# Performance work log

Hardware: AMD Instinct MI355X
Metric: run time of the kernel (lower is better)

Reference implementation:

```python
import jax, jax.numpy as jnp
import numpy as np

D = 384
EPS = 1e-12  # F.normalize eps


def setup_inputs() -> dict:
    key = jax.random.key(0)
    ks = jax.random.split(key, 12)
    s = 1.0 / np.sqrt(D)  # torch Linear default init scale
    return {
        "x": jax.random.normal(ks[0], (8192, D), jnp.float32),
        "y": jax.random.normal(ks[1], (8192, D), jnp.float32),
        "Wq": jax.random.uniform(ks[2], (D, D), jnp.float32, -s, s),
        "bq": jax.random.uniform(ks[3], (D,), jnp.float32, -s, s),
        "Wk": jax.random.uniform(ks[4], (D, D), jnp.float32, -s, s),
        "bk": jax.random.uniform(ks[5], (D,), jnp.float32, -s, s),
        "Wv": jax.random.uniform(ks[6], (D, D), jnp.float32, -s, s),
        "bv": jax.random.uniform(ks[7], (D,), jnp.float32, -s, s),
        "Wo": jax.random.uniform(ks[8], (D, D), jnp.float32, -s, s),
        "bo": jax.random.uniform(ks[9], (D,), jnp.float32, -s, s),
    }


def reference(x, y, Wq, bq, Wk, bk, Wv, bv, Wo, bo):
    # Q: [N, d], K/V: [M, d]
    Q = x @ Wq.T + bq
    K = y @ Wk.T + bk
    V = y @ Wv.T + bv
    scale = 1.0 / jnp.sqrt(jnp.asarray(Q.shape[-1], Q.dtype))
    attn = jax.nn.softmax((Q @ K.T) * scale, axis=-1)  # [N, M]
    ctx = attn @ V  # [N, d]
    # F.normalize(p=2, dim=1): divide by max(||row||_2, eps)
    norm = jnp.maximum(jnp.linalg.norm(ctx, axis=1, keepdims=True), EPS)
    ctx = ctx / norm
    return (x + ctx) @ Wo.T + bo
```

## Files before the change

### kernel.cpp

```cpp
#include <hip/hip_runtime.h>
#include <stdint.h>


typedef __attribute__((ext_vector_type(8))) short bf16x8;
typedef __attribute__((ext_vector_type(4))) float f32x4;
typedef __attribute__((ext_vector_type(16))) float f32x16;

#define DEV static __device__ __forceinline__

DEV short f2bf(float f) {
  uint32_t u = __builtin_bit_cast(uint32_t, f);
  u += 0x7fffu + ((u >> 16) & 1u);
  return (short)(u >> 16);
}
DEV uint32_t pack2(float a, float b) {
  return (uint32_t)(uint16_t)f2bf(a) | ((uint32_t)(uint16_t)f2bf(b) << 16);
}
DEV unsigned cvt_pk(float lo, float hi) {
  unsigned r;
  asm("v_cvt_pk_bf16_f32 %0, %1, %2" : "=v"(r) : "v"(lo), "v"(hi));
  return r;
}
DEV void pl32swap(unsigned& a, unsigned& b) {
  asm volatile("v_permlane32_swap_b32 %0, %1" : "+v"(a), "+v"(b));
}
DEV void gload16(const void* g, void* l) {
  __builtin_amdgcn_global_load_lds(
      (const __attribute__((address_space(1))) unsigned*)g,
      (__attribute__((address_space(3))) unsigned*)l, 16, 0, 0);
}

template <int BIAS_ON_N, int OUT_F32, int A_F32>
__global__ __launch_bounds__(256) void gemm_nt(
    const void* __restrict__ Aptr, const float* __restrict__ B,
    const float* __restrict__ bias, void* __restrict__ Cptr,
    int M, int N, int K, float scale) {
  __shared__ char As[128 * 128];
  __shared__ char Bs[128 * 128];
  const int tid = threadIdx.x;
  const int l = tid & 63, w = tid >> 6;
  const int lq = l & 15, lk = l >> 4;
  const int m0 = blockIdx.x * 128, n0 = blockIdx.y * 128;
  const int wr = (w >> 1) * 64, wc = (w & 1) * 64;
  f32x4 acc[4][4] = {};

  for (int k0 = 0; k0 < K; k0 += 64) {
    if (A_F32) {
      const float* A = (const float*)Aptr;
#pragma unroll
      for (int i = 0; i < 8; i++) {
        int c = tid + i * 256;
        int row = c >> 4, col = (c & 15) * 4;
        f32x4 v = *(const f32x4*)(A + (size_t)(m0 + row) * K + k0 + col);
        uint32_t lo = pack2(v.x, v.y), hi = pack2(v.z, v.w);
        int off = (row * 128 + col * 2) ^ ((row & 7) << 4);
        *(uint32_t*)(As + off) = lo;
        *(uint32_t*)(As + off + 4) = hi;
      }
    } else {
      const short* A = (const short*)Aptr;
#pragma unroll
      for (int i = 0; i < 4; i++) {
        int c = tid + i * 256;
        int row = c >> 3, col = (c & 7) * 8;
        uint4 v = *(const uint4*)(A + (size_t)(m0 + row) * K + k0 + col);
        int off = (row * 128 + col * 2) ^ ((row & 7) << 4);
        *(uint4*)(As + off) = v;
      }
    }
#pragma unroll
    for (int i = 0; i < 8; i++) {
      int c = tid + i * 256;
      int row = c >> 4, col = (c & 15) * 4;
      f32x4 v = *(const f32x4*)(B + (size_t)(n0 + row) * K + k0 + col);
      uint32_t lo = pack2(v.x, v.y), hi = pack2(v.z, v.w);
      int off = (row * 128 + col * 2) ^ ((row & 7) << 4);
      *(uint32_t*)(Bs + off) = lo;
      *(uint32_t*)(Bs + off + 4) = hi;
    }
    __syncthreads();
#pragma unroll
    for (int ks = 0; ks < 2; ks++) {
      bf16x8 af[4], bfr[4];
#pragma unroll
      for (int m = 0; m < 4; m++) {
        int row = wr + m * 16 + lq;
        af[m] = *(const bf16x8*)(As + ((row * 128 + ks * 64 + lk * 16) ^ ((row & 7) << 4)));
      }
#pragma unroll
      for (int n = 0; n < 4; n++) {
        int row = wc + n * 16 + lq;
        bfr[n] = *(const bf16x8*)(Bs + ((row * 128 + ks * 64 + lk * 16) ^ ((row & 7) << 4)));
      }
#pragma unroll
      for (int m = 0; m < 4; m++)
#pragma unroll
        for (int n = 0; n < 4; n++)
          acc[m][n] = __builtin_amdgcn_mfma_f32_16x16x32_bf16(af[m], bfr[n], acc[m][n], 0, 0, 0);
    }
    __syncthreads();
  }
#pragma unroll
  for (int m = 0; m < 4; m++) {
    int mg = m0 + wr + m * 16 + lk * 4;
#pragma unroll
    for (int n = 0; n < 4; n++) {
      int ng = n0 + wc + n * 16 + lq;
#pragma unroll
      for (int r = 0; r < 4; r++) {
        float v = (acc[m][n][r] + (BIAS_ON_N ? bias[ng] : bias[mg + r])) * scale;
        if (OUT_F32)
          ((float*)Cptr)[(size_t)(mg + r) * N + ng] = v;
        else
          ((short*)Cptr)[(size_t)(mg + r) * N + ng] = f2bf(v);
      }
    }
  }
}

#define ITERS 64

__global__ __launch_bounds__(256)
__attribute__((amdgpu_waves_per_eu(2, 2))) void flash_attn(
    const short* __restrict__ Qb, const short* __restrict__ Kb,
    const short* __restrict__ Vt, float* __restrict__ ctx_part) {
  __shared__ char Ks[2][24576];
  __shared__ char Vs[24576];
  const int tid = threadIdx.x, l = tid & 63, w = tid >> 6;
  const int l31 = l & 31, h = l >> 5;
  const int qh = w >> 1, dh = w & 1;
  const int sp = blockIdx.x & 3, qt = blockIdx.x >> 2;
  const int q0 = qt * 64 + qh * 32;
  const int kvbase = sp * 2048;

  int koff[6], voff[6];
#pragma unroll
  for (int i = 0; i < 6; i++) {
    int d = (w * 6 + i) * 1024 + l * 16;
    int krow = d / 768, kc = d - krow * 768;
    koff[i] = krow * 768 + (kc ^ ((krow & 7) << 4));
    int vrow = d >> 6, vc = d & 63;
    voff[i] = vrow * 16384 + (vc ^ (((vrow >> 1) & 3) << 4));
  }
  const int ldsoff = w * 6144 + 0;

  bf16x8 qf[24];
  {
    const short* qrow = Qb + (size_t)(q0 + l31) * 384 + h * 8;
#pragma unroll
    for (int s = 0; s < 24; s++) qf[s] = *(const bf16x8*)(qrow + s * 16);
  }
  asm volatile("s_waitcnt vmcnt(0)" ::: "memory");

  {
    const char* kb = (const char*)Kb + (size_t)kvbase * 768;
#pragma unroll
    for (int i = 0; i < 6; i++)
      gload16(kb + koff[i], (char*)Ks[0] + ldsoff + i * 1024);
  }

  f32x16 acc[6] = {};

#pragma unroll 1
  for (int t = 0; t < ITERS; t++) {
    const char* Kc = Ks[t & 1];
    {
      const char* vb = (const char*)Vt + (size_t)(kvbase + t * 32) * 2;
#pragma unroll
      for (int i = 0; i < 6; i++)
        gload16(vb + voff[i], Vs + ldsoff + i * 1024);
    }
    asm volatile("s_waitcnt vmcnt(6)" ::: "memory");
    __builtin_amdgcn_s_barrier();

    f32x16 S = {};
    const char* kcb = Kc + l31 * 768;
    const int swzk = (l31 & 7) << 4;
    __builtin_amdgcn_s_setprio(1);
#pragma unroll
    for (int s = 0; s < 24; s++) {
      bf16x8 k0 = *(const bf16x8*)(kcb + ((s * 32 + h * 16) ^ swzk));
      S = __builtin_amdgcn_mfma_f32_32x32x16_bf16(k0, qf[s], S, 0, 0, 0);
    }
    __builtin_amdgcn_s_setprio(0);

    if (t < ITERS - 1) {
      const char* kb = (const char*)Kb + (size_t)(kvbase + (t + 1) * 32) * 768;
      char* Kn = (char*)Ks[(t & 1) ^ 1];
#pragma unroll
      for (int i = 0; i < 6; i++)
        gload16(kb + koff[i], Kn + ldsoff + i * 1024);
    }

    unsigned a0 = cvt_pk(__builtin_amdgcn_exp2f(S[0]), __builtin_amdgcn_exp2f(S[1]));
    unsigned a1 = cvt_pk(__builtin_amdgcn_exp2f(S[2]), __builtin_amdgcn_exp2f(S[3]));
    unsigned a2 = cvt_pk(__builtin_amdgcn_exp2f(S[4]), __builtin_amdgcn_exp2f(S[5]));
    unsigned a3 = cvt_pk(__builtin_amdgcn_exp2f(S[6]), __builtin_amdgcn_exp2f(S[7]));
    pl32swap(a0, a2); pl32swap(a1, a3);
    uint4 pw0 = {a0, a1, a2, a3};
    bf16x8 pf0 = __builtin_bit_cast(bf16x8, pw0);
    unsigned b0 = cvt_pk(__builtin_amdgcn_exp2f(S[8]), __builtin_amdgcn_exp2f(S[9]));
    unsigned b1 = cvt_pk(__builtin_amdgcn_exp2f(S[10]), __builtin_amdgcn_exp2f(S[11]));
    unsigned b2 = cvt_pk(__builtin_amdgcn_exp2f(S[12]), __builtin_amdgcn_exp2f(S[13]));
    unsigned b3 = cvt_pk(__builtin_amdgcn_exp2f(S[14]), __builtin_amdgcn_exp2f(S[15]));
    pl32swap(b0, b2); pl32swap(b1, b3);
    uint4 pw1 = {b0, b1, b2, b3};
    bf16x8 pf1 = __builtin_bit_cast(bf16x8, pw1);

    if (t < ITERS - 1)
      asm volatile("s_waitcnt vmcnt(6)" ::: "memory");
    else
      asm volatile("s_waitcnt vmcnt(0)" ::: "memory");
    __builtin_amdgcn_s_barrier();

    const char* vsb = Vs + (dh * 192 + l31) * 64;
    __builtin_amdgcn_s_setprio(1);
#pragma unroll
    for (int nf = 0; nf < 6; nf++) {
      int vr = dh * 192 + nf * 32 + l31;
      int swz = ((vr >> 1) & 3) << 4;
      bf16x8 v0 = *(const bf16x8*)(vsb + nf * 2048 + ((h * 16) ^ swz));
      bf16x8 v1 = *(const bf16x8*)(vsb + nf * 2048 + ((32 + h * 16) ^ swz));
      acc[nf] = __builtin_amdgcn_mfma_f32_32x32x16_bf16(v0, pf0, acc[nf], 0, 0, 0);
      acc[nf] = __builtin_amdgcn_mfma_f32_32x32x16_bf16(v1, pf1, acc[nf], 0, 0, 0);
    }
    __builtin_amdgcn_s_setprio(0);
    __builtin_amdgcn_s_barrier();
  }

  float* outp = ctx_part + (size_t)sp * 8192 * 384 + (size_t)(q0 + l31) * 384;
#pragma unroll
  for (int nf = 0; nf < 6; nf++) {
#pragma unroll
    for (int qd = 0; qd < 4; qd++) {
      f32x4 v = {acc[nf][qd * 4 + 0], acc[nf][qd * 4 + 1],
                 acc[nf][qd * 4 + 2], acc[nf][qd * 4 + 3]};
      *(f32x4*)(outp + dh * 192 + nf * 32 + qd * 8 + h * 4) = v;
    }
  }
}

__global__ __launch_bounds__(256) void combine_norm(
    const float* __restrict__ ctx_part, const float* __restrict__ x,
    short* __restrict__ Xn) {
  const int l = threadIdx.x & 63, w = threadIdx.x >> 6;
  const int q = blockIdx.x * 4 + w;
  const size_t SLAB = (size_t)8192 * 384;
  float v[6];
  float ss = 0.f;
#pragma unroll
  for (int i = 0; i < 6; i++) {
    size_t off = (size_t)q * 384 + i * 64 + l;
    float s = ctx_part[off] + ctx_part[off + SLAB] + ctx_part[off + 2 * SLAB] +
              ctx_part[off + 3 * SLAB];
    v[i] = s;
    ss += s * s;
  }
#pragma unroll
  for (int m = 1; m <= 32; m <<= 1) ss += __shfl_xor(ss, m);
  float inv = 1.0f / fmaxf(sqrtf(ss), 1e-12f);
#pragma unroll
  for (int i = 0; i < 6; i++) {
    size_t off = (size_t)q * 384 + i * 64 + l;
    Xn[off] = f2bf(x[off] + v[i] * inv);
  }
}

extern "C" void kernel_launch(void* const* d_in, const int* in_sizes, int n_in,
                              void* d_out, int out_size, void* d_ws, size_t ws_size,
                              hipStream_t stream) {
  (void)in_sizes; (void)n_in; (void)out_size; (void)ws_size;
  const float* x  = (const float*)d_in[0];
  const float* y  = (const float*)d_in[1];
  const float* Wq = (const float*)d_in[2];
  const float* bq = (const float*)d_in[3];
  const float* Wk = (const float*)d_in[4];
  const float* bk = (const float*)d_in[5];
  const float* Wv = (const float*)d_in[6];
  const float* bv = (const float*)d_in[7];
  const float* Wo = (const float*)d_in[8];
  const float* bo = (const float*)d_in[9];

  char* ws = (char*)d_ws;
  short* Qb = (short*)(ws);
  short* Kb = (short*)(ws + 6291456);
  short* Vt = (short*)(ws + 12582912);
  short* Xn = (short*)(ws + 18874368);
  float* ctx = (float*)(ws + 25165824);

  const float SC = 0.07362233f;
  dim3 blk(256);
  gemm_nt<1, 0, 1><<<dim3(64, 3), blk, 0, stream>>>(x, Wq, bq, Qb, 8192, 384, 384, SC);
  gemm_nt<1, 0, 1><<<dim3(64, 3), blk, 0, stream>>>(y, Wk, bk, Kb, 8192, 384, 384, 1.0f);
  gemm_nt<0, 0, 1><<<dim3(3, 64), blk, 0, stream>>>(Wv, y, bv, Vt, 384, 8192, 384, 1.0f);
  flash_attn<<<dim3(512), blk, 0, stream>>>(Qb, Kb, Vt, ctx);
  combine_norm<<<dim3(2048), blk, 0, stream>>>(ctx, x, Xn);
  gemm_nt<1, 1, 0><<<dim3(64, 3), blk, 0, stream>>>(Xn, Wo, bo, (float*)d_out, 8192, 384, 384, 1.0f);
}
```

Baseline: 363.5 us.

## Split flash attention waves into alternating QK and PV roles with LDS-shared P

Doubles the flash attention block to 512 threads covering 128 queries, with half the waves loading K and half loading V. The two wave groups take turns computing QK^T/exp for a tile and pass the bf16 probabilities through shared memory. PV for tile t-1 runs while QK for tile t runs, using triple-buffered V and double-buffered P. This aims to overlap the two matmul stages and halve redundant QK work per query. In exchange it adds a full barrier per iteration, more LDS use and fewer blocks.

```diff
diff --git a/kernel.cpp b/kernel.cpp
--- a/kernel.cpp
+++ b/kernel.cpp
@@ -120,29 +120,39 @@
 
 #define ITERS 64
 
-__global__ __launch_bounds__(256)
+__global__ __launch_bounds__(512)
 __attribute__((amdgpu_waves_per_eu(2, 2))) void flash_attn(
     const short* __restrict__ Qb, const short* __restrict__ Kb,
     const short* __restrict__ Vt, float* __restrict__ ctx_part) {
   __shared__ char Ks[2][24576];
-  __shared__ char Vs[24576];
+  __shared__ char Vs[3][24576];
+  __shared__ char Ps[2][4][2048];
   const int tid = threadIdx.x, l = tid & 63, w = tid >> 6;
   const int l31 = l & 31, h = l >> 5;
-  const int qh = w >> 1, dh = w & 1;
+  const int qh = w & 3, dh = w >> 2;
   const int sp = blockIdx.x & 3, qt = blockIdx.x >> 2;
-  const int q0 = qt * 64 + qh * 32;
+  const int q0 = qt * 128 + qh * 32;
   const int kvbase = sp * 2048;
-
-  int koff[6], voff[6];
-#pragma unroll
-  for (int i = 0; i < 6; i++) {
-    int d = (w * 6 + i) * 1024 + l * 16;
-    int krow = d / 768, kc = d - krow * 768;
-    koff[i] = krow * 768 + (kc ^ ((krow & 7) << 4));
-    int vrow = d >> 6, vc = d & 63;
-    voff[i] = vrow * 16384 + (vc ^ (((vrow >> 1) & 3) << 4));
-  }
-  const int ldsoff = w * 6144 + 0;
+  const int pswz = ((l31 >> 2) & 7) << 4;
+  const int poff = (l31 * 32 + h * 16) ^ pswz;
+
+  int off6[6];
+  const int cb = (w & 3) * 6144;
+  if (dh == 0) {
+#pragma unroll
+    for (int i = 0; i < 6; i++) {
+      int d = cb + i * 1024 + l * 16;
+      int krow = d / 768, kc = d - krow * 768;
+      off6[i] = krow * 768 + (kc ^ ((krow & 7) << 4));
+    }
+  } else {
+#pragma unroll
+    for (int i = 0; i < 6; i++) {
+      int d = cb + i * 1024 + l * 16;
+      int vrow = d >> 6, vc = d & 63;
+      off6[i] = vrow * 16384 + (vc ^ (((vrow >> 1) & 3) << 4));
+    }
+  }
 
   bf16x8 qf[24];
   {
@@ -150,82 +160,101 @@
 #pragma unroll
     for (int s = 0; s < 24; s++) qf[s] = *(const bf16x8*)(qrow + s * 16);
   }
-  asm volatile("s_waitcnt vmcnt(0)" ::: "memory");
-
-  {
+
+  if (dh == 0) {
     const char* kb = (const char*)Kb + (size_t)kvbase * 768;
 #pragma unroll
-    for (int i = 0; i < 6; i++)
-      gload16(kb + koff[i], (char*)Ks[0] + ldsoff + i * 1024);
+    for (int i = 0; i < 6; i++) gload16(kb + off6[i], Ks[0] + cb + i * 1024);
+  } else {
+    const char* vb = (const char*)Vt + (size_t)kvbase * 2;
+#pragma unroll
+    for (int i = 0; i < 6; i++) gload16(vb + off6[i], Vs[0] + cb + i * 1024);
   }
 
   f32x16 acc[6] = {};
+  __syncthreads();
 
 #pragma unroll 1
   for (int t = 0; t < ITERS; t++) {
-    const char* Kc = Ks[t & 1];
-    {
-      const char* vb = (const char*)Vt + (size_t)(kvbase + t * 32) * 2;
-#pragma unroll
-      for (int i = 0; i < 6; i++)
-        gload16(vb + voff[i], Vs + ldsoff + i * 1024);
-    }
-    asm volatile("s_waitcnt vmcnt(6)" ::: "memory");
-    __builtin_amdgcn_s_barrier();
-
-    f32x16 S = {};
-    const char* kcb = Kc + l31 * 768;
-    const int swzk = (l31 & 7) << 4;
-    __builtin_amdgcn_s_setprio(1);
-#pragma unroll
-    for (int s = 0; s < 24; s++) {
-      bf16x8 k0 = *(const bf16x8*)(kcb + ((s * 32 + h * 16) ^ swzk));
-      S = __builtin_amdgcn_mfma_f32_32x32x16_bf16(k0, qf[s], S, 0, 0, 0);
-    }
-    __builtin_amdgcn_s_setprio(0);
-
     if (t < ITERS - 1) {
-      const char* kb = (const char*)Kb + (size_t)(kvbase + (t + 1) * 32) * 768;
-      char* Kn = (char*)Ks[(t & 1) ^ 1];
-#pragma unroll
-      for (int i = 0; i < 6; i++)
-        gload16(kb + koff[i], Kn + ldsoff + i * 1024);
-    }
-
-    unsigned a0 = cvt_pk(__builtin_amdgcn_exp2f(S[0]), __builtin_amdgcn_exp2f(S[1]));
-    unsigned a1 = cvt_pk(__builtin_amdgcn_exp2f(S[2]), __builtin_amdgcn_exp2f(S[3]));
-    unsigned a2 = cvt_pk(__builtin_amdgcn_exp2f(S[4]), __builtin_amdgcn_exp2f(S[5]));
-    unsigned a3 = cvt_pk(__builtin_amdgcn_exp2f(S[6]), __builtin_amdgcn_exp2f(S[7]));
-    pl32swap(a0, a2); pl32swap(a1, a3);
-    uint4 pw0 = {a0, a1, a2, a3};
-    bf16x8 pf0 = __builtin_bit_cast(bf16x8, pw0);
-    unsigned b0 = cvt_pk(__builtin_amdgcn_exp2f(S[8]), __builtin_amdgcn_exp2f(S[9]));
-    unsigned b1 = cvt_pk(__builtin_amdgcn_exp2f(S[10]), __builtin_amdgcn_exp2f(S[11]));
-    unsigned b2 = cvt_pk(__builtin_amdgcn_exp2f(S[12]), __builtin_amdgcn_exp2f(S[13]));
-    unsigned b3 = cvt_pk(__builtin_amdgcn_exp2f(S[14]), __builtin_amdgcn_exp2f(S[15]));
-    pl32swap(b0, b2); pl32swap(b1, b3);
-    uint4 pw1 = {b0, b1, b2, b3};
-    bf16x8 pf1 = __builtin_bit_cast(bf16x8, pw1);
-
-    if (t < ITERS - 1)
-      asm volatile("s_waitcnt vmcnt(6)" ::: "memory");
-    else
-      asm volatile("s_waitcnt vmcnt(0)" ::: "memory");
-    __builtin_amdgcn_s_barrier();
-
-    const char* vsb = Vs + (dh * 192 + l31) * 64;
-    __builtin_amdgcn_s_setprio(1);
+      int kv0 = kvbase + (t + 1) * 32;
+      if (dh == 0) {
+        const char* kb = (const char*)Kb + (size_t)kv0 * 768;
+        char* dst = Ks[(t + 1) & 1] + cb;
+#pragma unroll
+        for (int i = 0; i < 6; i++) gload16(kb + off6[i], dst + i * 1024);
+      } else {
+        const char* vb = (const char*)Vt + (size_t)kv0 * 2;
+        char* dst = Vs[(t + 1) % 3] + cb;
+#pragma unroll
+        for (int i = 0; i < 6; i++) gload16(vb + off6[i], dst + i * 1024);
+      }
+    }
+
+    if (dh == (t & 1)) {
+      f32x16 S = {};
+      const char* kcb = Ks[t & 1] + l31 * 768;
+      const int swzk = (l31 & 7) << 4;
+      __builtin_amdgcn_s_setprio(1);
+#pragma unroll
+      for (int s = 0; s < 24; s++) {
+        bf16x8 k0 = *(const bf16x8*)(kcb + ((s * 32 + h * 16) ^ swzk));
+        S = __builtin_amdgcn_mfma_f32_32x32x16_bf16(k0, qf[s], S, 0, 0, 0);
+      }
+      __builtin_amdgcn_s_setprio(0);
+      unsigned a0 = cvt_pk(__builtin_amdgcn_exp2f(S[0]), __builtin_amdgcn_exp2f(S[1]));
+      unsigned a1 = cvt_pk(__builtin_amdgcn_exp2f(S[2]), __builtin_amdgcn_exp2f(S[3]));
+      unsigned a2 = cvt_pk(__builtin_amdgcn_exp2f(S[4]), __builtin_amdgcn_exp2f(S[5]));
+      unsigned a3 = cvt_pk(__builtin_amdgcn_exp2f(S[6]), __builtin_amdgcn_exp2f(S[7]));
+      pl32swap(a0, a2); pl32swap(a1, a3);
+      uint4 pw0 = {a0, a1, a2, a3};
+      unsigned b0 = cvt_pk(__builtin_amdgcn_exp2f(S[8]), __builtin_amdgcn_exp2f(S[9]));
+      unsigned b1 = cvt_pk(__builtin_amdgcn_exp2f(S[10]), __builtin_amdgcn_exp2f(S[11]));
+      unsigned b2 = cvt_pk(__builtin_amdgcn_exp2f(S[12]), __builtin_amdgcn_exp2f(S[13]));
+      unsigned b3 = cvt_pk(__builtin_amdgcn_exp2f(S[14]), __builtin_amdgcn_exp2f(S[15]));
+      pl32swap(b0, b2); pl32swap(b1, b3);
+      uint4 pw1 = {b0, b1, b2, b3};
+      char* pwb = Ps[t & 1][qh];
+      *(uint4*)(pwb + poff) = pw0;
+      *(uint4*)(pwb + 1024 + poff) = pw1;
+    }
+
+    if (t > 0) {
+      const char* pb = Ps[(t - 1) & 1][qh];
+      bf16x8 pf0 = *(const bf16x8*)(pb + poff);
+      bf16x8 pf1 = *(const bf16x8*)(pb + 1024 + poff);
+      const char* vb = Vs[(t - 1) % 3];
+      __builtin_amdgcn_s_setprio(1);
+#pragma unroll
+      for (int nf = 0; nf < 6; nf++) {
+        int vr = dh * 192 + nf * 32 + l31;
+        int swz = ((vr >> 1) & 3) << 4;
+        const char* vrow = vb + vr * 64;
+        bf16x8 v0 = *(const bf16x8*)(vrow + ((h * 16) ^ swz));
+        bf16x8 v1 = *(const bf16x8*)(vrow + ((32 + h * 16) ^ swz));
+        acc[nf] = __builtin_amdgcn_mfma_f32_32x32x16_bf16(v0, pf0, acc[nf], 0, 0, 0);
+        acc[nf] = __builtin_amdgcn_mfma_f32_32x32x16_bf16(v1, pf1, acc[nf], 0, 0, 0);
+      }
+      __builtin_amdgcn_s_setprio(0);
+    }
+    __syncthreads();
+  }
+
+  {
+    const char* pb = Ps[(ITERS - 1) & 1][qh];
+    bf16x8 pf0 = *(const bf16x8*)(pb + poff);
+    bf16x8 pf1 = *(const bf16x8*)(pb + 1024 + poff);
+    const char* vb = Vs[(ITERS - 1) % 3];
 #pragma unroll
     for (int nf = 0; nf < 6; nf++) {
       int vr = dh * 192 + nf * 32 + l31;
       int swz = ((vr >> 1) & 3) << 4;
-      bf16x8 v0 = *(const bf16x8*)(vsb + nf * 2048 + ((h * 16) ^ swz));
-      bf16x8 v1 = *(const bf16x8*)(vsb + nf * 2048 + ((32 + h * 16) ^ swz));
+      const char* vrow = vb + vr * 64;
+      bf16x8 v0 = *(const bf16x8*)(vrow + ((h * 16) ^ swz));
+      bf16x8 v1 = *(const bf16x8*)(vrow + ((32 + h * 16) ^ swz));
       acc[nf] = __builtin_amdgcn_mfma_f32_32x32x16_bf16(v0, pf0, acc[nf], 0, 0, 0);
       acc[nf] = __builtin_amdgcn_mfma_f32_32x32x16_bf16(v1, pf1, acc[nf], 0, 0, 0);
     }
-    __builtin_amdgcn_s_setprio(0);
-    __builtin_amdgcn_s_barrier();
   }
 
   float* outp = ctx_part + (size_t)sp * 8192 * 384 + (size_t)(q0 + l31) * 384;
@@ -293,7 +322,7 @@
   gemm_nt<1, 0, 1><<<dim3(64, 3), blk, 0, stream>>>(x, Wq, bq, Qb, 8192, 384, 384, SC);
   gemm_nt<1, 0, 1><<<dim3(64, 3), blk, 0, stream>>>(y, Wk, bk, Kb, 8192, 384, 384, 1.0f);
   gemm_nt<0, 0, 1><<<dim3(3, 64), blk, 0, stream>>>(Wv, y, bv, Vt, 384, 8192, 384, 1.0f);
-  flash_attn<<<dim3(512), blk, 0, stream>>>(Qb, Kb, Vt, ctx);
+  flash_attn<<<dim3(256), dim3(512), 0, stream>>>(Qb, Kb, Vt, ctx);
   combine_norm<<<dim3(2048), blk, 0, stream>>>(ctx, x, Xn);
   gemm_nt<1, 1, 0><<<dim3(64, 3), blk, 0, stream>>>(Xn, Wo, bo, (float*)d_out, 8192, 384, 384, 1.0f);
 }
```

After: 302.0 us. -16.9%, faster.
